# Optimization experiments

Measured on AMD Instinct MI355X. Metric: run time of the kernel, lower is better.

The kernel has to match this reference:

```python
import jax, jax.numpy as jnp
import numpy as np

DIM = 768
HEADS = 12
HEAD_DIM = DIM // HEADS
SCALE = HEAD_DIM ** (-0.5)
BATCH = 1
SEQ = 4096


def setup_inputs() -> dict:
    key = jax.random.key(0)
    ks = jax.random.split(key, 5)
    x = jax.random.normal(ks[0], (BATCH, SEQ, DIM), dtype=jnp.float32)
    # Linear params stored (in, out) for y = x @ W + b
    w_qkv = jax.random.normal(ks[1], (DIM, 3 * DIM), dtype=jnp.float32) * (DIM ** -0.5)
    b_qkv = jnp.zeros((3 * DIM,), dtype=jnp.float32)
    w_proj = jax.random.normal(ks[2], (DIM, DIM), dtype=jnp.float32) * (DIM ** -0.5)
    b_proj = jnp.zeros((DIM,), dtype=jnp.float32)
    return {"x": x, "w_qkv": w_qkv, "b_qkv": b_qkv, "w_proj": w_proj, "b_proj": b_proj}


def reference(x, w_qkv, b_qkv, w_proj, b_proj):
    B, S, _ = x.shape
    qkv = x @ w_qkv + b_qkv                              # [B,S,3*DIM]
    qkv = qkv.reshape(B, S, 3, HEADS, HEAD_DIM)
    q, k, v = qkv[:, :, 0], qkv[:, :, 1], qkv[:, :, 2]   # [B,S,H,D]
    # scaled dot-product attention, full score matrix as in the original
    attn = jnp.einsum("bqhd,bkhd->bhqk", q * SCALE, k)   # [B,H,S,S]
    attn = jax.nn.softmax(attn, axis=-1)
    out = jnp.einsum("bhqk,bkhd->bqhd", attn, v)         # [B,S,H,D]
    out = out.reshape(B, S, DIM)
    return out @ w_proj + b_proj
```

## Files before the change

### kernel.cpp

```cpp
#include <hip/hip_runtime.h>
#include <hip/hip_bf16.h>

#define SEQ   4096
#define DIM   768
#define HEADS 12
#define NQKV  2304
#define QSCALE 0.18033688011f

#if __has_builtin(__builtin_amdgcn_exp2f)
#define EXP2(x) __builtin_amdgcn_exp2f(x)
#else
#define EXP2(x) __expf((x) * 0.69314718056f)
#endif

typedef __bf16 bf16_t;
typedef bf16_t bf16x8 __attribute__((ext_vector_type(8)));
typedef float  f32x4  __attribute__((ext_vector_type(4)));
typedef float  f32x16 __attribute__((ext_vector_type(16)));
typedef unsigned short u16;
typedef unsigned int   u32;

static __device__ __forceinline__ float bf2f(u16 v) {
    union { float f; unsigned u; } x; x.u = ((unsigned)v) << 16; return x.f;
}
static __device__ __forceinline__ u16 f2bf(float f) {
    union { float f; unsigned u; } x; x.f = f;
    unsigned r = x.u + 0x7fff + ((x.u >> 16) & 1);
    return (u16)(r >> 16);
}
static __device__ __forceinline__ u32 fbits(float f) {
    union { float f; unsigned u; } x; x.f = f; return x.u;
}
static __device__ __forceinline__ void gload_lds16(const u16* g, u16* l) {
    __builtin_amdgcn_global_load_lds(
        (const __attribute__((address_space(1))) unsigned int*)g,
        (__attribute__((address_space(3))) unsigned int*)l, 16, 0, 0);
}

static __device__ __forceinline__ int detect_f32(const u32* __restrict__ x) {
    int lane = threadIdx.x & 63;
    int cnt = 0;
#pragma unroll
    for (int i = 0; i < 8; ++i) {
        u32 w = x[lane * 8 + i];
        cnt += (((w >> 7) & 0xFF) >= 0x8F) ? 1 : 0;
    }
#pragma unroll
    for (int m = 1; m < 64; m <<= 1) cnt += __shfl_xor(cnt, m);
    return cnt >= 64;
}

__global__ __launch_bounds__(256) void prep(
    const void* __restrict__ x, const void* __restrict__ wqkv,
    const void* __restrict__ bqkv, const void* __restrict__ wproj,
    const void* __restrict__ bproj,
    u16* __restrict__ cvt, u16* __restrict__ wqkvT, u16* __restrict__ wprojT)
{
    __shared__ u16 tile[64][65];
    const bool f32 = detect_f32((const u32*)x) != 0;
    const int b = blockIdx.x;
    const int t = threadIdx.x;

    if (b < 576) {
        const void* src; u16* dst; int K, N, tx, ty;
        if (b < 432) { src = wqkv; dst = wqkvT; K = DIM; N = NQKV; tx = b % 36; ty = b / 36; }
        else { int bb = b - 432; src = wproj; dst = wprojT; K = DIM; N = DIM; tx = bb % 12; ty = bb / 12; }
        const int k0 = ty * 64, n0 = tx * 64;
#pragma unroll
        for (int i = 0; i < 16; ++i) {
            int idx = i * 256 + t;
            int r = idx >> 6, c = idx & 63;
            size_t si = (size_t)(k0 + r) * N + n0 + c;
            tile[r][c] = f32 ? f2bf(((const float*)src)[si]) : ((const u16*)src)[si];
        }
        __syncthreads();
#pragma unroll
        for (int i = 0; i < 16; ++i) {
            int idx = i * 256 + t;
            int r = idx >> 6, c = idx & 63;
            dst[(size_t)(n0 + r) * K + k0 + c] = tile[c][r];
        }
    } else {
        const int SX = SEQ * DIM, e1 = SX + NQKV;
        const int n_cvt = e1 + DIM;
        for (int i = (b - 576) * 256 + t; i < n_cvt; i += 200 * 256) {
            const void* s; int off;
            if      (i < SX) { s = x; off = i; }
            else if (i < e1) { s = bqkv; off = i - SX; }
            else             { s = bproj; off = i - e1; }
            cvt[i] = f32 ? f2bf(((const float*)s)[off]) : ((const u16*)s)[off];
        }
    }
}

template<int MODE>
__global__ __launch_bounds__(256) void gemm128(
    const u16* __restrict__ A, const u16* __restrict__ BT, const u16* __restrict__ bias,
    u16* __restrict__ C0, float* __restrict__ Cf, u16* __restrict__ VT,
    const u32* __restrict__ xdet, int M, int N, int K)
{
    __shared__ u16 a_lds[128 * 32];
    __shared__ u16 b_lds[128 * 32];

    const int t    = threadIdx.x;
    const int w    = t >> 6;
    const int lane = t & 63;
    const int l15  = lane & 15;
    const int quad = lane >> 4;
    const int wm   = w >> 1, wn = w & 1;
    const int m0   = blockIdx.y * 128, n0 = blockIdx.x * 128;

    const int srow = w * 32 + (lane >> 2);
    const int kch  = (lane & 3) * 8;
    const u16* asrc = A  + (size_t)(m0 + srow) * K + kch;
    const u16* bsrc = BT + (size_t)(n0 + srow) * K + kch;
    u16* adst = a_lds + w * 32 * 32;
    u16* bdst = b_lds + w * 32 * 32;

    f32x4 acc[4][4] = {};

    for (int kt = 0; kt < K; kt += 32) {
        __syncthreads();
        gload_lds16(asrc,          adst);
        gload_lds16(asrc + 16 * K, adst + 16 * 32);
        gload_lds16(bsrc,          bdst);
        gload_lds16(bsrc + 16 * K, bdst + 16 * 32);
        asrc += 32; bsrc += 32;
        __syncthreads();

        const u16* ab = a_lds + (wm * 64 + l15) * 32 + quad * 8;
        const u16* bb = b_lds + (wn * 64 + l15) * 32 + quad * 8;
        bf16x8 af[4], bfr[4];
#pragma unroll
        for (int i = 0; i < 4; ++i) af[i]  = *(const bf16x8*)(ab + i * 16 * 32);
#pragma unroll
        for (int j = 0; j < 4; ++j) bfr[j] = *(const bf16x8*)(bb + j * 16 * 32);
#pragma unroll
        for (int i = 0; i < 4; ++i)
#pragma unroll
            for (int j = 0; j < 4; ++j)
                acc[i][j] = __builtin_amdgcn_mfma_f32_16x16x32_bf16(af[i], bfr[j], acc[i][j], 0, 0, 0);
    }

    bool outf32 = false;
    if (MODE == 0) outf32 = detect_f32(xdet) != 0;
#pragma unroll
    for (int i = 0; i < 4; ++i)
#pragma unroll
        for (int j = 0; j < 4; ++j)
#pragma unroll
            for (int r = 0; r < 4; ++r) {
                int m = m0 + wm * 64 + i * 16 + quad * 4 + r;
                int n = n0 + wn * 64 + j * 16 + l15;
                float v = acc[i][j][r] + bf2f(bias[n]);
                if (MODE == 0) {
                    if (outf32) Cf[(size_t)m * N + n] = v;
                    else        C0[(size_t)m * N + n] = f2bf(v);
                } else {
                    if (n < 768) {
                        C0[(size_t)m * 1536 + n] = f2bf(v * QSCALE);
                    } else if (n < 1536) {
                        C0[(size_t)m * 1536 + n] = f2bf(v);
                    } else {
                        int mp = (m & ~15) | (m & 3) |
                                 (((m >> 2) & 1) << 3) | (((m >> 3) & 1) << 2);
                        VT[(size_t)(n - 1536) * SEQ + mp] = f2bf(v);
                    }
                }
            }
}

__global__ __launch_bounds__(256) void attn_kernel(
    const u16* __restrict__ qk, const u16* __restrict__ vt, u16* __restrict__ out)
{
    __shared__ u16 k_lds[2][64 * 64];
    __shared__ u16 v_lds[2][64 * 64];
    __shared__ float l_red[2][2][32];

    const int t    = threadIdx.x;
    const int w    = t >> 6;
    const int lane = t & 63;
    const int l31  = lane & 31;
    const int h    = lane >> 5;
    const int wq   = w & 1;
    const int wk   = w >> 1;
    const int head = blockIdx.y;
    const int q0   = blockIdx.x * 64 + wq * 32;

    const u16* qrow = qk + (size_t)(q0 + l31) * 1536 + head * 64 + h * 8;
    bf16x8 qb[4];
#pragma unroll
    for (int s = 0; s < 4; ++s) qb[s] = *(const bf16x8*)(qrow + 16 * s);

    bf16x8 ones;
#pragma unroll
    for (int j = 0; j < 8; ++j) ones[j] = (bf16_t)1.0f;

    const int srow = 8 * w + (lane >> 3);
    const int cs   = ((lane & 7) - srow) & 7;
    const u16* kg = qk + 768 + head * 64 + (size_t)srow * 1536 + cs * 8;
    const u16* vg = vt + (size_t)head * 64 * SEQ + (size_t)srow * SEQ + cs * 8;
    const int woff = 8 * w * 64;

    const int krow = 32 * wk + l31;

    f32x16 o0 = {}, o1 = {}, lac = {};

    auto stage = [&](u16* kd, u16* vd, int T) {
        const u16* kgT = kg + (size_t)T * 64 * 1536;
        const u16* vgT = vg + (size_t)T * 64;
        gload_lds16(kgT,                      kd + woff);
        gload_lds16(kgT + (size_t)32 * 1536,  kd + woff + 32 * 64);
        gload_lds16(vgT,                      vd + woff);
        gload_lds16(vgT + (size_t)32 * SEQ,   vd + woff + 32 * 64);
    };

    auto compute = [&](const u16* kb, const u16* vb) {
        f32x16 st = {};
#pragma unroll
        for (int s = 0; s < 4; ++s) {
            bf16x8 ka = *(const bf16x8*)(kb + krow * 64 + (((2 * s + h + krow) & 7) * 8));
            st = __builtin_amdgcn_mfma_f32_32x32x16_bf16(ka, qb[s], st, 0, 0, 0);
        }
        u32 q32[8];
#pragma unroll
        for (int i = 0; i < 8; ++i) {
            float pe = EXP2(st[2 * i]);
            float po = EXP2(st[2 * i + 1]);
            q32[i] = __builtin_amdgcn_perm(fbits(po), fbits(pe), 0x07060302u);
        }
        union { u32 u[4]; bf16x8 v; } pf0, pf1;
#pragma unroll
        for (int i = 0; i < 4; ++i) { pf0.u[i] = q32[i]; pf1.u[i] = q32[4 + i]; }
#pragma unroll
        for (int s2 = 0; s2 < 2; ++s2) {
            const int c = 4 * wk + 2 * s2 + h;
            bf16x8 vb0 = *(const bf16x8*)(vb + l31 * 64 + (((c + l31) & 7) * 8));
            bf16x8 vb1 = *(const bf16x8*)(vb + (32 + l31) * 64 + (((c + 32 + l31) & 7) * 8));
            const bf16x8 pv = s2 ? pf1.v : pf0.v;
            o0  = __builtin_amdgcn_mfma_f32_32x32x16_bf16(pv, vb0, o0, 0, 0, 0);
            o1  = __builtin_amdgcn_mfma_f32_32x32x16_bf16(pv, vb1, o1, 0, 0, 0);
            lac = __builtin_amdgcn_mfma_f32_32x32x16_bf16(pv, ones, lac, 0, 0, 0);
        }
    };

    stage(&k_lds[0][0], &v_lds[0][0], 0);
    __syncthreads();
    for (int T = 0; T < 64; T += 2) {
        stage(&k_lds[1][0], &v_lds[1][0], T + 1);
        compute(&k_lds[0][0], &v_lds[0][0]);
        __syncthreads();
        if (T + 2 < 64) stage(&k_lds[0][0], &v_lds[0][0], T + 2);
        compute(&k_lds[1][0], &v_lds[1][0]);
        __syncthreads();
    }

    if (l31 == 0) {
#pragma unroll
        for (int r = 0; r < 16; ++r) {
            int row = (r & 3) + 8 * (r >> 2) + 4 * h;
            l_red[wq][wk][row] = lac[r];
        }
    }
    float* scr = (wq == 0) ? (float*)&k_lds[0][0] : (float*)&v_lds[0][0];
    if (wk == 1) {
#pragma unroll
        for (int r = 0; r < 16; ++r) {
            int row = (r & 3) + 8 * (r >> 2) + 4 * h;
            scr[row * 64 + l31]      = o0[r];
            scr[row * 64 + 32 + l31] = o1[r];
        }
    }
    __syncthreads();
    if (wk == 0) {
#pragma unroll
        for (int r = 0; r < 16; ++r) {
            int row = (r & 3) + 8 * (r >> 2) + 4 * h;
            float lt   = l_red[wq][0][row] + l_red[wq][1][row];
            float invl = 1.0f / lt;
            float s0 = o0[r] + scr[row * 64 + l31];
            float s1 = o1[r] + scr[row * 64 + 32 + l31];
            size_t gr = (size_t)(q0 + row) * 768 + head * 64;
            out[gr + l31]      = f2bf(s0 * invl);
            out[gr + 32 + l31] = f2bf(s1 * invl);
        }
    }
}

extern "C" void kernel_launch(void* const* d_in, const int* in_sizes, int n_in,
                              void* d_out, int out_size, void* d_ws, size_t ws_size,
                              hipStream_t stream) {
    const int SX = SEQ * DIM;

    u16* base   = (u16*)d_ws;
    u16* xb     = base;
    u16* bqkvb  = xb + SX;
    u16* bprojb = bqkvb + NQKV;
    u16* wqkvT  = bprojb + DIM;
    u16* wprojT = wqkvT + (size_t)NQKV * DIM;
    u16* qkb    = wprojT + (size_t)DIM * DIM;
    u16* vtb    = qkb + (size_t)SEQ * 1536;
    u16* attnb  = xb;

    prep<<<776, 256, 0, stream>>>(
        d_in[0], d_in[1], d_in[2], d_in[3], d_in[4], base, wqkvT, wprojT);
    gemm128<1><<<dim3(NQKV / 128, SEQ / 128), 256, 0, stream>>>(
        xb, wqkvT, bqkvb, qkb, nullptr, vtb, (const u32*)d_in[0],
        SEQ, NQKV, DIM);
    attn_kernel<<<dim3(SEQ / 64, HEADS), 256, 0, stream>>>(qkb, vtb, attnb);
    gemm128<0><<<dim3(DIM / 128, SEQ / 128), 256, 0, stream>>>(
        attnb, wprojT, bprojb, (u16*)d_out, (float*)d_out, nullptr,
        (const u32*)d_in[0], SEQ, DIM, DIM);
}
```

Before: 233.6 us.

## Triple-buffer K/V tiles with counted vmcnt waits, setprio, and remapped block order

The attention main loop moves from a double buffer with full __syncthreads to a three-stage LDS ring. Partial vmcnt waits keep two tile loads in flight while the current tile is computed, which is meant to hide global-to-LDS latency. It also raises wave priority around the MFMA sections and remaps block indices so consecutive blocks spread across heads, which should improve L2 locality across XCDs. The cost is 50% more LDS per block, which may lower occupancy, and the correctness of the hand-written vmcnt(4) counting depends on the exact number of loads issued per stage.

```diff
diff --git a/kernel.cpp b/kernel.cpp
--- a/kernel.cpp
+++ b/kernel.cpp
@@ -173,8 +173,8 @@
 __global__ __launch_bounds__(256) void attn_kernel(
     const u16* __restrict__ qk, const u16* __restrict__ vt, u16* __restrict__ out)
 {
-    __shared__ u16 k_lds[2][64 * 64];
-    __shared__ u16 v_lds[2][64 * 64];
+    __shared__ u16 k_lds[3][64 * 64];
+    __shared__ u16 v_lds[3][64 * 64];
     __shared__ float l_red[2][2][32];
 
     const int t    = threadIdx.x;
@@ -184,8 +184,11 @@
     const int h    = lane >> 5;
     const int wq   = w & 1;
     const int wk   = w >> 1;
-    const int head = blockIdx.y;
-    const int q0   = blockIdx.x * 64 + wq * 32;
+
+    const int lin     = blockIdx.x + (blockIdx.y << 6);
+    const int logical = (lin & 7) * 96 + (lin >> 3);
+    const int head    = logical >> 6;
+    const int q0      = (logical & 63) * 64 + wq * 32;
 
     const u16* qrow = qk + (size_t)(q0 + l31) * 1536 + head * 64 + h * 8;
     bf16x8 qb[4];
@@ -217,11 +220,13 @@
 
     auto compute = [&](const u16* kb, const u16* vb) {
         f32x16 st = {};
+        __builtin_amdgcn_s_setprio(1);
 #pragma unroll
         for (int s = 0; s < 4; ++s) {
             bf16x8 ka = *(const bf16x8*)(kb + krow * 64 + (((2 * s + h + krow) & 7) * 8));
             st = __builtin_amdgcn_mfma_f32_32x32x16_bf16(ka, qb[s], st, 0, 0, 0);
         }
+        __builtin_amdgcn_s_setprio(0);
         u32 q32[8];
 #pragma unroll
         for (int i = 0; i < 8; ++i) {
@@ -232,6 +237,7 @@
         union { u32 u[4]; bf16x8 v; } pf0, pf1;
 #pragma unroll
         for (int i = 0; i < 4; ++i) { pf0.u[i] = q32[i]; pf1.u[i] = q32[4 + i]; }
+        __builtin_amdgcn_s_setprio(1);
 #pragma unroll
         for (int s2 = 0; s2 < 2; ++s2) {
             const int c = 4 * wk + 2 * s2 + h;
@@ -242,18 +248,29 @@
             o1  = __builtin_amdgcn_mfma_f32_32x32x16_bf16(pv, vb1, o1, 0, 0, 0);
             lac = __builtin_amdgcn_mfma_f32_32x32x16_bf16(pv, ones, lac, 0, 0, 0);
         }
+        __builtin_amdgcn_s_setprio(0);
     };
 
-    stage(&k_lds[0][0], &v_lds[0][0], 0);
+    u16 *kA = &k_lds[0][0], *kB = &k_lds[1][0], *kC = &k_lds[2][0];
+    u16 *vA = &v_lds[0][0], *vB = &v_lds[1][0], *vC = &v_lds[2][0];
+
+    stage(kA, vA, 0);
+    stage(kB, vB, 1);
+    for (int T = 0; T < 62; ++T) {
+        asm volatile("s_waitcnt vmcnt(4)" ::: "memory");
+        __builtin_amdgcn_s_barrier();
+        stage(kC, vC, T + 2);
+        compute(kA, vA);
+        u16* tk = kA; kA = kB; kB = kC; kC = tk;
+        u16* tv = vA; vA = vB; vB = vC; vC = tv;
+    }
+    asm volatile("s_waitcnt vmcnt(4)" ::: "memory");
+    __builtin_amdgcn_s_barrier();
+    compute(kA, vA);
+    asm volatile("s_waitcnt vmcnt(0)" ::: "memory");
+    __builtin_amdgcn_s_barrier();
+    compute(kB, vB);
     __syncthreads();
-    for (int T = 0; T < 64; T += 2) {
-        stage(&k_lds[1][0], &v_lds[1][0], T + 1);
-        compute(&k_lds[0][0], &v_lds[0][0]);
-        __syncthreads();
-        if (T + 2 < 64) stage(&k_lds[0][0], &v_lds[0][0], T + 2);
-        compute(&k_lds[1][0], &v_lds[1][0]);
-        __syncthreads();
-    }
 
     if (l31 == 0) {
 #pragma unroll
```

New measurement: 232.4 us. Within noise of the previous version (-0.5%).
